# Kernel optimization log

Measured on AMD Instinct MI355X. Metric: run time of the kernel, lower is better.

Reference implementation:

```python
import jax, jax.numpy as jnp
import numpy as np

IN_DIM = 1024
HID = 256
OUT_DIM = 1000
NUM_BINS = 51
BATCH = 2048
N_LEGAL = 200


def setup_inputs() -> dict:
    key = jax.random.key(0)
    ks = jax.random.split(key, 12)
    s = lambda fan_in: 1.0 / np.sqrt(fan_in)
    u = lambda k, shp, b: jax.random.uniform(k, shp, jnp.float32, -b, b)
    return {
        "x": jax.random.normal(ks[0], (BATCH, IN_DIM), jnp.float32),
        # weights stored as [in, out] (math-equivalent to torch Linear)
        "w_in": u(ks[1], (IN_DIM, HID), s(IN_DIM)),
        "b_in": u(ks[2], (HID,), s(IN_DIM)),
        "w_ah": u(ks[3], (HID, HID), s(HID)),
        "b_ah": u(ks[4], (HID,), s(HID)),
        "w_ao": u(ks[5], (HID, OUT_DIM * NUM_BINS), s(HID)),
        "b_ao": u(ks[6], (OUT_DIM * NUM_BINS,), s(HID)),
        "w_vh": u(ks[7], (HID, HID), s(HID)),
        "b_vh": u(ks[8], (HID,), s(HID)),
        "w_vo": u(ks[9], (HID, NUM_BINS), s(HID)),
        "b_vo": u(ks[10], (NUM_BINS,), s(HID)),
        "v_range": jnp.linspace(-10.0, 10.0, NUM_BINS, dtype=jnp.float32),
        "possible_moves": jax.random.randint(ks[11], (BATCH, N_LEGAL), 0, OUT_DIM),
    }


def reference(x, w_in, b_in, w_ah, b_ah, w_ao, b_ao, w_vh, b_vh, w_vo, b_vo,
              v_range, possible_moves):
    B = x.shape[0]
    h = jax.nn.relu(x @ w_in + b_in)                       # [B, 256]
    adv_h = jax.nn.relu(h @ w_ah + b_ah)                   # [B, 256]
    val_h = jax.nn.relu(h @ w_vh + b_vh)                   # [B, 256]
    adv = (adv_h @ w_ao + b_ao).reshape(B, OUT_DIM, NUM_BINS)
    val = (val_h @ w_vo + b_vo).reshape(B, 1, NUM_BINS)
    q = val + adv - adv.mean(axis=1, keepdims=True)        # [B, A, bins]
    p = jnp.maximum(jax.nn.softmax(q, axis=2), 1e-5)       # softmax + clamp(min=1e-5)
    q_vals = jnp.sum(p * v_range, axis=2)                  # [B, A]
    # LegalSoftmax: per-row scatter of 1.0 at legal indices, vectorized
    mask = jnp.zeros((B, OUT_DIM), x.dtype).at[
        jnp.arange(B)[:, None], possible_moves].set(1.0)
    filtered = q_vals * mask
    # faithful to torch: any exact-zero entry (masked OR coincidental) -> -inf
    return jnp.where(filtered == 0, -jnp.inf, filtered)
```

## Files before the change

### kernel.cpp

```cpp
#include <hip/hip_runtime.h>
#include <cstdint>
#include <cstddef>

#define NB      2048
#define INDIM   1024
#define HID     256
#define NA      1000
#define BINS    51
#define NLEG    200
#define NPAIR   (NB*NLEG)
#define PPB     (NPAIR/256)
#define RSTRIDE 768

#define NEG_SENTINEL (-1.0e30f)

typedef float    f32x4  __attribute__((ext_vector_type(4)));
typedef __bf16   bf16x8 __attribute__((ext_vector_type(8)));
typedef unsigned short us8 __attribute__((ext_vector_type(8)));
typedef unsigned short us4 __attribute__((ext_vector_type(4)));
typedef unsigned long long u64x2 __attribute__((ext_vector_type(2)));

__device__ __forceinline__ unsigned short f2bf(float f) {
  union { float f; unsigned u; } v; v.f = f;
  return (unsigned short)((v.u + 0x7FFFu + ((v.u >> 16) & 1u)) >> 16);
}
__device__ __forceinline__ bf16x8 as_bf(us8 v) { return __builtin_bit_cast(bf16x8, v); }
__device__ __forceinline__ int imin(int a, int b) { return a < b ? a : b; }

__device__ __forceinline__ unsigned f2fp8x4(float a, float b, float c, float d) {
  int v = 0;
  v = __builtin_amdgcn_cvt_pk_fp8_f32(a, b, v, false);
  v = __builtin_amdgcn_cvt_pk_fp8_f32(c, d, v, true);
  return (unsigned)v;
}
__device__ __forceinline__ unsigned char f2fp8(float f) {
  int v = __builtin_amdgcn_cvt_pk_fp8_f32(f, 0.f, 0, false);
  return (unsigned char)(v & 0xff);
}
__device__ __forceinline__ float fp82f(unsigned char u) {
  return __builtin_amdgcn_cvt_f32_fp8((int)u, 0);
}

__global__ __launch_bounds__(256) void k_pre(
    const float* __restrict__ w_ao, unsigned char* __restrict__ wp8,
    float* __restrict__ wmean_acc,
    const float* __restrict__ w_in, const float* __restrict__ w_ah,
    const float* __restrict__ w_vh,
    unsigned short* __restrict__ w_inT, unsigned short* __restrict__ w_ahT,
    unsigned short* __restrict__ w_vhT,
    float* __restrict__ out,
    const float* __restrict__ x, unsigned short* __restrict__ x_bf) {
  __shared__ __align__(16) unsigned char smem[16320];
  int b = blockIdx.x, tid = threadIdx.x;
  if (b < 1000) {
    unsigned char* st = smem;
    int s = b & 7, a0 = (b >> 3) * 8;
    const float* wbase = w_ao + (size_t)(s * 32) * (NA * BINS) + a0 * BINS;
    for (int i = tid; i < 816; i += 256) {
      int kq = i / 102, c4 = i - kq * 102;
      const float* rp = wbase + (size_t)(kq * 4) * (NA * BINS) + c4 * 4;
      float4 f0 = *(const float4*)(rp);
      float4 f1 = *(const float4*)(rp + NA * BINS);
      float4 f2 = *(const float4*)(rp + 2 * NA * BINS);
      float4 f3 = *(const float4*)(rp + 3 * NA * BINS);
      unsigned pk0 = f2fp8x4(f0.x * 16.f, f0.y * 16.f, f0.z * 16.f, f0.w * 16.f);
      unsigned pk1 = f2fp8x4(f1.x * 16.f, f1.y * 16.f, f1.z * 16.f, f1.w * 16.f);
      unsigned pk2 = f2fp8x4(f2.x * 16.f, f2.y * 16.f, f2.z * 16.f, f2.w * 16.f);
      unsigned pk3 = f2fp8x4(f3.x * 16.f, f3.y * 16.f, f3.z * 16.f, f3.w * 16.f);
      unsigned s01lo = __builtin_amdgcn_perm(pk1, pk0, 0x05010400u);
      unsigned s01hi = __builtin_amdgcn_perm(pk1, pk0, 0x07030602u);
      unsigned s23lo = __builtin_amdgcn_perm(pk3, pk2, 0x05010400u);
      unsigned s23hi = __builtin_amdgcn_perm(pk3, pk2, 0x07030602u);
      unsigned o0 = __builtin_amdgcn_perm(s23lo, s01lo, 0x05040100u);
      unsigned o1 = __builtin_amdgcn_perm(s23lo, s01lo, 0x07060302u);
      unsigned o2 = __builtin_amdgcn_perm(s23hi, s01hi, 0x05040100u);
      unsigned o3 = __builtin_amdgcn_perm(s23hi, s01hi, 0x07060302u);
      int k4 = kq * 4;
      int swz = ((c4 >> 2) & 3) << 3;
      int kb = ((k4 & 24) ^ swz) + (k4 & 7);
      int cbase = c4 * 160;
      *(unsigned*)(st + cbase + kb)       = o0;
      *(unsigned*)(st + cbase + 40 + kb)  = o1;
      *(unsigned*)(st + cbase + 80 + kb)  = o2;
      *(unsigned*)(st + cbase + 120 + kb) = o3;
    }
    __syncthreads();
    for (int i = tid; i < 32 * 51; i += 256) {
      int r = i / 51, j = i - r * 51;
      float s8 = 0.f;
#pragma unroll
      for (int aL = 0; aL < 8; aL++) {
        int c = aL * 51 + j;
        s8 += fp82f(st[c * 40 + ((r & 24) ^ (((c >> 4) & 3) << 3)) + (r & 7)]);
      }
      atomicAdd(&wmean_acc[(size_t)(s * 32 + r) * BINS + j], s8);
    }
    int t4 = (tid >> 6) & 3, l = tid & 63;
    int col = t4 * 16 + (l & 15), kg = l >> 4;
    for (int aL = 0; aL < 8; aL++) {
      unsigned lo = 0, hi = 0;
      if (col < BINS) {
        int ci = aL * 51 + col;
        unsigned long long v8 = *(const unsigned long long*)(
            st + ci * 40 + ((kg * 8) ^ (((ci >> 4) & 3) << 3)));
        lo = (unsigned)v8; hi = (unsigned)(v8 >> 32);
      }
      uint2 v; v.x = lo; v.y = hi;
      *(uint2*)(wp8 + (size_t)(a0 + aL) * 16384 +
                (size_t)((s * 2 + (t4 >> 1)) * 64 + l) * 16 + (t4 & 1) * 8) = v;
    }
  } else if (b < 1384) {
    int bb = b - 1000;
    float (*tile)[33] = (float(*)[33])smem;
    const float* w; unsigned short* wT; int K, N, kt, nt;
    if (bb < 256)      { w = w_in; wT = w_inT; K = INDIM; N = HID; kt = bb & 31;        nt = bb >> 5; }
    else if (bb < 320) { w = w_ah; wT = w_ahT; K = HID;   N = HID; kt = (bb - 256) & 7; nt = (bb - 256) >> 3; }
    else               { w = w_vh; wT = w_vhT; K = HID;   N = HID; kt = (bb - 320) & 7; nt = (bb - 320) >> 3; }
    int k0 = kt * 32, n0 = nt * 32;
    int cr = tid >> 5, cc = tid & 31;
#pragma unroll
    for (int it = 0; it < 4; it++)
      tile[cr + it * 8][cc] = w[(size_t)(k0 + cr + it * 8) * N + n0 + cc];
    __syncthreads();
#pragma unroll
    for (int it = 0; it < 4; it++)
      wT[(size_t)(n0 + cr + it * 8) * K + k0 + cc] = f2bf(tile[cc][cr + it * 8]);
  } else if (b < 1884) {
    int base = (b - 1384) * 1024 + tid;
    float4 v = {NEG_SENTINEL, NEG_SENTINEL, NEG_SENTINEL, NEG_SENTINEL};
#pragma unroll
    for (int it = 0; it < 4; it++) ((float4*)out)[base + it * 256] = v;
  } else {
    int base4 = (b - 1884) * 1024 + tid;
#pragma unroll
    for (int it = 0; it < 4; it++) {
      float4 v = ((const float4*)x)[base4 + it * 256];
      us4 o;
      o[0] = f2bf(v.x); o[1] = f2bf(v.y); o[2] = f2bf(v.z); o[3] = f2bf(v.w);
      ((us4*)x_bf)[base4 + it * 256] = o;
    }
  }
}

__global__ __launch_bounds__(256) void k_mid(
    const unsigned short* __restrict__ x_bf, const unsigned short* __restrict__ w_inT,
    const float* __restrict__ b_in, unsigned short* __restrict__ h_bf,
    const float* __restrict__ w_vo, const float* __restrict__ wmean_acc,
    const float* __restrict__ b_vo, const float* __restrict__ b_ao,
    unsigned short* __restrict__ Wc, float* __restrict__ bias_c) {
  __shared__ __align__(16) char smem[1024];
  int b = blockIdx.x, tid = threadIdx.x;
  if (b < 512) {
    int w = tid >> 6, l = tid & 63, la = l & 15, g = l >> 4;
    int idx = b * 4 + w;
    int m0 = (idx & 127) * 16, n0 = (idx >> 7) * 16;
    f32x4 acc = {0.f, 0.f, 0.f, 0.f};
    const us8* Bp = (const us8*)(w_inT + (size_t)(n0 + la) * INDIM) + g;
    const us8* Ap = (const us8*)(x_bf + (size_t)(m0 + la) * INDIM) + g;
#pragma unroll 8
    for (int s = 0; s < 32; s++)
      acc = __builtin_amdgcn_mfma_f32_16x16x32_bf16(as_bf(Ap[s * 4]), as_bf(Bp[s * 4]),
                                                    acc, 0, 0, 0);
    float bb = b_in[n0 + la];
#pragma unroll
    for (int r = 0; r < 4; r++) {
      float v = fmaxf(acc[r] + bb, 0.f);
      h_bf[(size_t)(m0 + g * 4 + r) * HID + n0 + la] = f2bf(v);
    }
  } else {
    float* sred = (float*)smem;
    int n = b - 512, t = tid;
    for (int k = t; k < 512; k += 256) {
      float v = 0.f;
      if (n < BINS)
        v = (k < 256) ? w_vo[(size_t)k * BINS + n]
                      : (-(0.001f / 16.f) * wmean_acc[(size_t)(k - 256) * BINS + n]);
      Wc[(size_t)n * 512 + k] = f2bf(v);
    }
    float acc = 0.f;
    if (n < BINS)
      for (int a = t; a < NA; a += 256) acc += b_ao[(size_t)a * BINS + n];
    sred[t] = acc;
    __syncthreads();
    for (int d = 128; d > 0; d >>= 1) { if (t < d) sred[t] += sred[t + d]; __syncthreads(); }
    if (t == 0) bias_c[n] = (n < BINS) ? (b_vo[n] - 0.001f * sred[0]) : 0.f;
  }
}

__global__ __launch_bounds__(256) void k_heads(
    const unsigned short* __restrict__ h,
    const unsigned short* __restrict__ wA, const float* __restrict__ bA,
    const unsigned short* __restrict__ wV, const float* __restrict__ bV,
    const unsigned short* __restrict__ Wc, const float* __restrict__ bias_c,
    unsigned char* __restrict__ Aext8, float* __restrict__ cbuf_f,
    const int* __restrict__ pm, int* __restrict__ cursor, int* __restrict__ rows) {
  __shared__ __align__(16) char smem[16896];
  int b = blockIdx.x, tid = threadIdx.x;
  if (b < 128) {
    unsigned short* aL = (unsigned short*)smem;
    unsigned short* vL = (unsigned short*)smem + 16 * 264;
    int w = tid >> 6, l = tid & 63, la = l & 15, g = l >> 4;
    int m0 = b * 16;
    const us8* Ap = (const us8*)(h + (size_t)(m0 + la) * HID) + g;
    us8 aF[8];
#pragma unroll
    for (int s = 0; s < 8; s++) aF[s] = Ap[s * 4];
#pragma unroll
    for (int part = 0; part < 2; part++) {
      const unsigned short* BT = part ? wV : wA;
      const float* bias = part ? bV : bA;
      unsigned short* oL = part ? vL : aL;
#pragma unroll
      for (int nt = 0; nt < 4; nt++) {
        int n0 = w * 64 + nt * 16;
        f32x4 acc = {0.f, 0.f, 0.f, 0.f};
        const us8* Bp = (const us8*)(BT + (size_t)(n0 + la) * HID) + g;
#pragma unroll
        for (int s = 0; s < 8; s++)
          acc = __builtin_amdgcn_mfma_f32_16x16x32_bf16(as_bf(aF[s]), as_bf(Bp[s * 4]),
                                                        acc, 0, 0, 0);
        float bb = bias[n0 + la];
#pragma unroll
        for (int r = 0; r < 4; r++) {
          float v = fmaxf(acc[r] + bb, 0.f);
          oL[(g * 4 + r) * 264 + n0 + la] = f2bf(v);
          if (part == 0)
            Aext8[(size_t)(m0 + g * 4 + r) * HID + n0 + la] = f2fp8(v);
        }
      }
    }
    __syncthreads();
    int n0c = w * 16;
    f32x4 acc = {0.f, 0.f, 0.f, 0.f};
    const us8* Vp  = (const us8*)(vL + la * 264) + g;
    const us8* Ap2 = (const us8*)(aL + la * 264) + g;
    const us8* BpV = (const us8*)(Wc + (size_t)(n0c + la) * 512) + g;
    const us8* BpA = (const us8*)(Wc + (size_t)(n0c + la) * 512 + 256) + g;
#pragma unroll
    for (int s = 0; s < 8; s++)
      acc = __builtin_amdgcn_mfma_f32_16x16x32_bf16(as_bf(Vp[s * 4]), as_bf(BpV[s * 4]),
                                                    acc, 0, 0, 0);
#pragma unroll
    for (int s = 0; s < 8; s++)
      acc = __builtin_amdgcn_mfma_f32_16x16x32_bf16(as_bf(Ap2[s * 4]), as_bf(BpA[s * 4]),
                                                    acc, 0, 0, 0);
    float bb = bias_c[n0c + la];
#pragma unroll
    for (int r = 0; r < 4; r++)
      cbuf_f[(size_t)(m0 + g * 4 + r) * 64 + n0c + la] = acc[r] + bb;
  } else {
    int* lc = (int*)smem;
    int* lbase = (int*)(smem + 4096);
    int blk = b - 128, t = tid;
    for (int i = t; i < NA; i += 256) lc[i] = 0;
    __syncthreads();
    int pbase = blk * PPB;
    for (int i = t; i < PPB; i += 256) atomicAdd(&lc[pm[pbase + i]], 1);
    __syncthreads();
    for (int i = t; i < NA; i += 256) {
      int v = lc[i];
      lbase[i] = v ? atomicAdd(&cursor[i], v) : 0;
      lc[i] = 0;
    }
    __syncthreads();
    for (int i = t; i < PPB; i += 256) {
      int a = pm[pbase + i];
      int r = atomicAdd(&lc[a], 1);
      rows[(size_t)a * RSTRIDE + lbase[a] + r] = (pbase + i) / NLEG;
    }
  }
}

#define TILE_BODY(TILE, RA_) do {                                              \
  int rA = (RA_);                                                              \
  const long long* Ap = (const long long*)(Aext8 + (size_t)rA * HID) + g;      \
  const float4* cf = (const float4*)(cbuf_f + (size_t)rA * 64);                \
  long long a8[8];                                                             \
  _Pragma("unroll") for (int s = 0; s < 8; s++) a8[s] = Ap[s * 4];             \
  float4 cq0 = cf[g], cq1 = cf[4 + g], cq2 = cf[8 + g], cq3 = cf[12 + g];      \
  f32x4 acc0 = {0.f,0.f,0.f,0.f}, acc1 = {0.f,0.f,0.f,0.f};                    \
  f32x4 acc2 = {0.f,0.f,0.f,0.f}, acc3 = {0.f,0.f,0.f,0.f};                    \
  __builtin_amdgcn_s_setprio(1);                                               \
  _Pragma("unroll") for (int s = 0; s < 8; s++) {                              \
    u64x2 b01 = sBv[(s * 2) * 64 + l];                                         \
    u64x2 b23 = sBv[(s * 2 + 1) * 64 + l];                                     \
    acc0 = __builtin_amdgcn_mfma_f32_16x16x32_fp8_fp8(                         \
        (long long)b01[0], a8[s], acc0, 0, 0, 0);                              \
    acc1 = __builtin_amdgcn_mfma_f32_16x16x32_fp8_fp8(                         \
        (long long)b01[1], a8[s], acc1, 0, 0, 0);                              \
    acc2 = __builtin_amdgcn_mfma_f32_16x16x32_fp8_fp8(                         \
        (long long)b23[0], a8[s], acc2, 0, 0, 0);                              \
    acc3 = __builtin_amdgcn_mfma_f32_16x16x32_fp8_fp8(                         \
        (long long)b23[1], a8[s], acc3, 0, 0, 0);                              \
  }                                                                            \
  __builtin_amdgcn_s_setprio(0);                                               \
  float S = 0.f;                                                               \
  f32x4 e0, e1, e2, e3;                                                        \
  _Pragma("unroll") for (int r = 0; r < 4; r++) {                              \
    e0[r] = __expf(fmaf(acc0[r], 0.0625f, cq0[r] + bao0[r])); S += e0[r];      \
    e1[r] = __expf(fmaf(acc1[r], 0.0625f, cq1[r] + bao1[r])); S += e1[r];      \
    e2[r] = __expf(fmaf(acc2[r], 0.0625f, cq2[r] + bao2[r])); S += e2[r];      \
    e3[r] = __expf(fmaf(acc3[r], 0.0625f, cq3[r] + bao3[r])); S += e3[r];      \
  }                                                                            \
  S += __shfl_xor(S, 16); S += __shfl_xor(S, 32);                              \
  float inv = 1.f / S, qv = 0.f;                                               \
  _Pragma("unroll") for (int r = 0; r < 4; r++) {                              \
    int bin = g * 4 + r;                                                       \
    qv = fmaf(fmaxf(e0[r] * inv, 1e-5f), (float)bin * 0.4f - 10.f, qv);        \
    qv = fmaf(fmaxf(e1[r] * inv, 1e-5f), (float)(bin + 16) * 0.4f - 10.f, qv); \
    qv = fmaf(fmaxf(e2[r] * inv, 1e-5f), (float)(bin + 32) * 0.4f - 10.f, qv); \
    if (bin + 48 < BINS)                                                       \
      qv = fmaf(fmaxf(e3[r] * inv, 1e-5f), (float)(bin + 48) * 0.4f - 10.f, qv); \
  }                                                                            \
  qv += __shfl_xor(qv, 16); qv += __shfl_xor(qv, 32);                          \
  int gi = (TILE) * 16 + la;                                                   \
  if (g == 0 && gi < count)                                                    \
    out[(size_t)rA * NA + a] = (qv == 0.f) ? NEG_SENTINEL : qv;                \
} while (0)

__global__ __launch_bounds__(256) void k_main_mfma(
    const unsigned char* __restrict__ Aext8,
    const float* __restrict__ cbuf_f,
    const unsigned char* __restrict__ wp8,
    const float* __restrict__ b_ao,
    const int* __restrict__ cnt,
    const int* __restrict__ rows,
    float* __restrict__ out) {
  __shared__ __align__(16) long long sB8[2048];
  const u64x2* sBv = (const u64x2*)sB8;
  int bx = blockIdx.x;
  int a = (bx & 7) * 125 + (bx >> 3);
  int count = cnt[a];
  int ntiles = (count + 15) >> 4;
  if (count == 0 || (int)(blockIdx.y * 4) >= ntiles) return;
  int tid = threadIdx.x;
  int w = tid >> 6, l = tid & 63, la = l & 15, g = l >> 4;
  int base = a * RSTRIDE;
  int t0 = blockIdx.y * 4 + w;

  int rQ0 = rows[base + imin( t0       * 16 + la, count - 1)];
  int rQ1 = rows[base + imin((t0 +  8) * 16 + la, count - 1)];
  int rQ2 = rows[base + imin((t0 + 16) * 16 + la, count - 1)];
  int rQ3 = rows[base + imin((t0 + 24) * 16 + la, count - 1)];

  const float* baop = b_ao + (size_t)a * BINS;
  f32x4 bao0, bao1, bao2, bao3;
#pragma unroll
  for (int r = 0; r < 4; r++) {
    int bin = g * 4 + r;
    bao0[r] = baop[bin];
    bao1[r] = baop[bin + 16];
    bao2[r] = baop[bin + 32];
    bao3[r] = (bin + 48 < BINS) ? baop[bin + 48] : NEG_SENTINEL;
  }

  const u64x2* wpa = (const u64x2*)(wp8 + (size_t)a * 16384);
#pragma unroll
  for (int i = 0; i < 4; i++) ((u64x2*)sB8)[tid + i * 256] = wpa[tid + i * 256];
  __syncthreads();

  if (t0      < ntiles) TILE_BODY(t0,      rQ0);
  if (t0 +  8 < ntiles) TILE_BODY(t0 +  8, rQ1);
  if (t0 + 16 < ntiles) TILE_BODY(t0 + 16, rQ2);
  if (t0 + 24 < ntiles) TILE_BODY(t0 + 24, rQ3);
  for (int tile = t0 + 32; tile < ntiles; tile += 8) {
    int rAt = rows[base + imin(tile * 16 + la, count - 1)];
    TILE_BODY(tile, rAt);
  }
}

extern "C" void kernel_launch(void* const* d_in, const int* in_sizes, int n_in,
                              void* d_out, int out_size, void* d_ws, size_t ws_size,
                              hipStream_t stream) {
  (void)in_sizes; (void)n_in; (void)out_size; (void)ws_size;
  const float* x     = (const float*)d_in[0];
  const float* w_in  = (const float*)d_in[1];
  const float* b_in  = (const float*)d_in[2];
  const float* w_ah  = (const float*)d_in[3];
  const float* b_ah  = (const float*)d_in[4];
  const float* w_ao  = (const float*)d_in[5];
  const float* b_ao  = (const float*)d_in[6];
  const float* w_vh  = (const float*)d_in[7];
  const float* b_vh  = (const float*)d_in[8];
  const float* w_vo  = (const float*)d_in[9];
  const float* b_vo  = (const float*)d_in[10];
  const int*   pm    = (const int*)d_in[12];
  float* out = (float*)d_out;

  char* p = (char*)d_ws;
  unsigned char*  wp8    = (unsigned char*)p;  p += (size_t)NA * 32 * 512;
  unsigned char*  Aext8  = (unsigned char*)p;  p += (size_t)NB * HID;
  unsigned short* h_bf   = (unsigned short*)p; p += (size_t)NB * HID * 2;
  unsigned short* w_inT  = (unsigned short*)p; p += (size_t)HID * INDIM * 2;
  unsigned short* w_ahT  = (unsigned short*)p; p += (size_t)HID * HID * 2;
  unsigned short* w_vhT  = (unsigned short*)p; p += (size_t)HID * HID * 2;
  unsigned short* Wc     = (unsigned short*)p; p += (size_t)64 * 512 * 2;
  unsigned short* x_bf   = (unsigned short*)p; p += (size_t)NB * INDIM * 2;
  float* bias_c = (float*)p; p += 64 * 4;
  float* cbuf_f = (float*)p; p += (size_t)NB * 64 * 4;
  float* wmean  = (float*)p; p += 13056 * 4;
  int* cursor = (int*)p; p += (size_t)NA * 4 + 240;
  int* rows   = (int*)p; p += (size_t)NA * RSTRIDE * 4 + 256;

  hipMemsetAsync(wmean, 0, (13056 + NA) * sizeof(float), stream);

  k_pre<<<2396, 256, 0, stream>>>(w_ao, wp8, wmean, w_in, w_ah, w_vh,
                                  w_inT, w_ahT, w_vhT, out, x, x_bf);
  k_mid<<<576, 256, 0, stream>>>(x_bf, w_inT, b_in, h_bf,
                                 w_vo, wmean, b_vo, b_ao, Wc, bias_c);
  k_heads<<<384, 256, 0, stream>>>(h_bf, w_ahT, b_ah, w_vhT, b_vh,
                                   Wc, bias_c, Aext8, cbuf_f,
                                   pm, cursor, rows);
  k_main_mfma<<<dim3(1000, 2), 256, 0, stream>>>(Aext8, cbuf_f, wp8, b_ao,
                                                 cursor, rows, out);
}
```

Before: 201.1 us.

## Spread column-mean atomics over slices and double-buffer row prefetch in main kernel

The weight-column-mean accumulation in k_pre now spreads its atomics across 25 partial buffers by slice, so fewer blocks contend on the same addresses. k_mid then sums the 25 slices when it builds Wc. In k_main_mfma the per-tile body is split into a prefetch macro and a compute macro, with two register sets (A/B), so the next tile's gathered A rows and cbuf loads are issued before the current tile's MFMA and softmax. This costs a larger memset and workspace, more reads in k_mid, and higher register pressure in the main kernel.

```diff
diff --git a/kernel.cpp b/kernel.cpp
--- a/kernel.cpp
+++ b/kernel.cpp
@@ -11,6 +11,7 @@
 #define NPAIR   (NB*NLEG)
 #define PPB     (NPAIR/256)
 #define RSTRIDE 768
+#define NSLICE  25
 
 #define NEG_SENTINEL (-1.0e30f)
 
@@ -43,7 +44,7 @@
 
 __global__ __launch_bounds__(256) void k_pre(
     const float* __restrict__ w_ao, unsigned char* __restrict__ wp8,
-    float* __restrict__ wmean_acc,
+    float* __restrict__ wpart,
     const float* __restrict__ w_in, const float* __restrict__ w_ah,
     const float* __restrict__ w_vh,
     unsigned short* __restrict__ w_inT, unsigned short* __restrict__ w_ahT,
@@ -85,6 +86,7 @@
       *(unsigned*)(st + cbase + 120 + kb) = o3;
     }
     __syncthreads();
+    int slice = (b >> 3) % NSLICE;
     for (int i = tid; i < 32 * 51; i += 256) {
       int r = i / 51, j = i - r * 51;
       float s8 = 0.f;
@@ -93,7 +95,7 @@
         int c = aL * 51 + j;
         s8 += fp82f(st[c * 40 + ((r & 24) ^ (((c >> 4) & 3) << 3)) + (r & 7)]);
       }
-      atomicAdd(&wmean_acc[(size_t)(s * 32 + r) * BINS + j], s8);
+      atomicAdd(&wpart[(size_t)slice * 13056 + (s * 32 + r) * 51 + j], s8);
     }
     int t4 = (tid >> 6) & 3, l = tid & 63;
     int col = t4 * 16 + (l & 15), kg = l >> 4;
@@ -145,7 +147,7 @@
 __global__ __launch_bounds__(256) void k_mid(
     const unsigned short* __restrict__ x_bf, const unsigned short* __restrict__ w_inT,
     const float* __restrict__ b_in, unsigned short* __restrict__ h_bf,
-    const float* __restrict__ w_vo, const float* __restrict__ wmean_acc,
+    const float* __restrict__ w_vo, const float* __restrict__ wpart,
     const float* __restrict__ b_vo, const float* __restrict__ b_ao,
     unsigned short* __restrict__ Wc, float* __restrict__ bias_c) {
   __shared__ __align__(16) char smem[1024];
@@ -172,9 +174,17 @@
     int n = b - 512, t = tid;
     for (int k = t; k < 512; k += 256) {
       float v = 0.f;
-      if (n < BINS)
-        v = (k < 256) ? w_vo[(size_t)k * BINS + n]
-                      : (-(0.001f / 16.f) * wmean_acc[(size_t)(k - 256) * BINS + n]);
+      if (n < BINS) {
+        if (k < 256) {
+          v = w_vo[(size_t)k * BINS + n];
+        } else {
+          float ssum = 0.f;
+#pragma unroll
+          for (int sl = 0; sl < NSLICE; sl++)
+            ssum += wpart[(size_t)sl * 13056 + (k - 256) * 51 + n];
+          v = -(0.001f / 16.f) * ssum;
+        }
+      }
       Wc[(size_t)n * 512 + k] = f2bf(v);
     }
     float acc = 0.f;
@@ -271,51 +281,58 @@
   }
 }
 
-#define TILE_BODY(TILE, RA_) do {                                              \
-  int rA = (RA_);                                                              \
-  const long long* Ap = (const long long*)(Aext8 + (size_t)rA * HID) + g;      \
-  const float4* cf = (const float4*)(cbuf_f + (size_t)rA * 64);                \
-  long long a8[8];                                                             \
-  _Pragma("unroll") for (int s = 0; s < 8; s++) a8[s] = Ap[s * 4];             \
-  float4 cq0 = cf[g], cq1 = cf[4 + g], cq2 = cf[8 + g], cq3 = cf[12 + g];      \
-  f32x4 acc0 = {0.f,0.f,0.f,0.f}, acc1 = {0.f,0.f,0.f,0.f};                    \
-  f32x4 acc2 = {0.f,0.f,0.f,0.f}, acc3 = {0.f,0.f,0.f,0.f};                    \
+#define PREF(P, RA_) do {                                                      \
+  rA##P = (RA_);                                                               \
+  const long long* Ap_ = (const long long*)(Aext8 + (size_t)rA##P * HID) + g;  \
+  a##P##0 = Ap_[0];  a##P##1 = Ap_[4];  a##P##2 = Ap_[8];  a##P##3 = Ap_[12];  \
+  a##P##4 = Ap_[16]; a##P##5 = Ap_[20]; a##P##6 = Ap_[24]; a##P##7 = Ap_[28];  \
+  const float4* cf_ = (const float4*)(cbuf_f + (size_t)rA##P * 64);            \
+  cq##P##0 = cf_[g];     cq##P##1 = cf_[4 + g];                                \
+  cq##P##2 = cf_[8 + g]; cq##P##3 = cf_[12 + g];                               \
+} while (0)
+
+#define MSTEP(P, S) do {                                                       \
+  u64x2 b01_ = sBv[(S * 2) * 64 + l];                                          \
+  u64x2 b23_ = sBv[(S * 2 + 1) * 64 + l];                                      \
+  acc0_ = __builtin_amdgcn_mfma_f32_16x16x32_fp8_fp8(                          \
+      (long long)b01_[0], a##P##S, acc0_, 0, 0, 0);                            \
+  acc1_ = __builtin_amdgcn_mfma_f32_16x16x32_fp8_fp8(                          \
+      (long long)b01_[1], a##P##S, acc1_, 0, 0, 0);                            \
+  acc2_ = __builtin_amdgcn_mfma_f32_16x16x32_fp8_fp8(                          \
+      (long long)b23_[0], a##P##S, acc2_, 0, 0, 0);                            \
+  acc3_ = __builtin_amdgcn_mfma_f32_16x16x32_fp8_fp8(                          \
+      (long long)b23_[1], a##P##S, acc3_, 0, 0, 0);                            \
+} while (0)
+
+#define COMP(P, TILE) do {                                                     \
+  f32x4 acc0_ = {0.f,0.f,0.f,0.f}, acc1_ = {0.f,0.f,0.f,0.f};                  \
+  f32x4 acc2_ = {0.f,0.f,0.f,0.f}, acc3_ = {0.f,0.f,0.f,0.f};                  \
   __builtin_amdgcn_s_setprio(1);                                               \
-  _Pragma("unroll") for (int s = 0; s < 8; s++) {                              \
-    u64x2 b01 = sBv[(s * 2) * 64 + l];                                         \
-    u64x2 b23 = sBv[(s * 2 + 1) * 64 + l];                                     \
-    acc0 = __builtin_amdgcn_mfma_f32_16x16x32_fp8_fp8(                         \
-        (long long)b01[0], a8[s], acc0, 0, 0, 0);                              \
-    acc1 = __builtin_amdgcn_mfma_f32_16x16x32_fp8_fp8(                         \
-        (long long)b01[1], a8[s], acc1, 0, 0, 0);                              \
-    acc2 = __builtin_amdgcn_mfma_f32_16x16x32_fp8_fp8(                         \
-        (long long)b23[0], a8[s], acc2, 0, 0, 0);                              \
-    acc3 = __builtin_amdgcn_mfma_f32_16x16x32_fp8_fp8(                         \
-        (long long)b23[1], a8[s], acc3, 0, 0, 0);                              \
+  MSTEP(P, 0); MSTEP(P, 1); MSTEP(P, 2); MSTEP(P, 3);                          \
+  MSTEP(P, 4); MSTEP(P, 5); MSTEP(P, 6); MSTEP(P, 7);                          \
+  __builtin_amdgcn_s_setprio(0);                                               \
+  float S_ = 0.f;                                                              \
+  f32x4 e0_, e1_, e2_, e3_;                                                    \
+  _Pragma("unroll") for (int r_ = 0; r_ < 4; r_++) {                           \
+    e0_[r_] = __expf(fmaf(acc0_[r_], 0.0625f, cq##P##0[r_] + bao0[r_])); S_ += e0_[r_]; \
+    e1_[r_] = __expf(fmaf(acc1_[r_], 0.0625f, cq##P##1[r_] + bao1[r_])); S_ += e1_[r_]; \
+    e2_[r_] = __expf(fmaf(acc2_[r_], 0.0625f, cq##P##2[r_] + bao2[r_])); S_ += e2_[r_]; \
+    e3_[r_] = __expf(fmaf(acc3_[r_], 0.0625f, cq##P##3[r_] + bao3[r_])); S_ += e3_[r_]; \
   }                                                                            \
-  __builtin_amdgcn_s_setprio(0);                                               \
-  float S = 0.f;                                                               \
-  f32x4 e0, e1, e2, e3;                                                        \
-  _Pragma("unroll") for (int r = 0; r < 4; r++) {                              \
-    e0[r] = __expf(fmaf(acc0[r], 0.0625f, cq0[r] + bao0[r])); S += e0[r];      \
-    e1[r] = __expf(fmaf(acc1[r], 0.0625f, cq1[r] + bao1[r])); S += e1[r];      \
-    e2[r] = __expf(fmaf(acc2[r], 0.0625f, cq2[r] + bao2[r])); S += e2[r];      \
-    e3[r] = __expf(fmaf(acc3[r], 0.0625f, cq3[r] + bao3[r])); S += e3[r];      \
+  S_ += __shfl_xor(S_, 16); S_ += __shfl_xor(S_, 32);                          \
+  float inv_ = 1.f / S_, qv_ = 0.f;                                            \
+  _Pragma("unroll") for (int r_ = 0; r_ < 4; r_++) {                           \
+    int bin_ = g * 4 + r_;                                                     \
+    qv_ = fmaf(fmaxf(e0_[r_] * inv_, 1e-5f), (float)bin_ * 0.4f - 10.f, qv_);  \
+    qv_ = fmaf(fmaxf(e1_[r_] * inv_, 1e-5f), (float)(bin_ + 16) * 0.4f - 10.f, qv_); \
+    qv_ = fmaf(fmaxf(e2_[r_] * inv_, 1e-5f), (float)(bin_ + 32) * 0.4f - 10.f, qv_); \
+    if (bin_ + 48 < BINS)                                                      \
+      qv_ = fmaf(fmaxf(e3_[r_] * inv_, 1e-5f), (float)(bin_ + 48) * 0.4f - 10.f, qv_); \
   }                                                                            \
-  S += __shfl_xor(S, 16); S += __shfl_xor(S, 32);                              \
-  float inv = 1.f / S, qv = 0.f;                                               \
-  _Pragma("unroll") for (int r = 0; r < 4; r++) {                              \
-    int bin = g * 4 + r;                                                       \
-    qv = fmaf(fmaxf(e0[r] * inv, 1e-5f), (float)bin * 0.4f - 10.f, qv);        \
-    qv = fmaf(fmaxf(e1[r] * inv, 1e-5f), (float)(bin + 16) * 0.4f - 10.f, qv); \
-    qv = fmaf(fmaxf(e2[r] * inv, 1e-5f), (float)(bin + 32) * 0.4f - 10.f, qv); \
-    if (bin + 48 < BINS)                                                       \
-      qv = fmaf(fmaxf(e3[r] * inv, 1e-5f), (float)(bin + 48) * 0.4f - 10.f, qv); \
-  }                                                                            \
-  qv += __shfl_xor(qv, 16); qv += __shfl_xor(qv, 32);                          \
-  int gi = (TILE) * 16 + la;                                                   \
-  if (g == 0 && gi < count)                                                    \
-    out[(size_t)rA * NA + a] = (qv == 0.f) ? NEG_SENTINEL : qv;                \
+  qv_ += __shfl_xor(qv_, 16); qv_ += __shfl_xor(qv_, 32);                      \
+  int gi_ = (TILE) * 16 + la;                                                  \
+  if (g == 0 && gi_ < count)                                                   \
+    out[(size_t)rA##P * NA + a] = (qv_ == 0.f) ? NEG_SENTINEL : qv_;           \
 } while (0)
 
 __global__ __launch_bounds__(256) void k_main_mfma(
@@ -359,13 +376,26 @@
   for (int i = 0; i < 4; i++) ((u64x2*)sB8)[tid + i * 256] = wpa[tid + i * 256];
   __syncthreads();
 
-  if (t0      < ntiles) TILE_BODY(t0,      rQ0);
-  if (t0 +  8 < ntiles) TILE_BODY(t0 +  8, rQ1);
-  if (t0 + 16 < ntiles) TILE_BODY(t0 + 16, rQ2);
-  if (t0 + 24 < ntiles) TILE_BODY(t0 + 24, rQ3);
+  int rAA, rAB;
+  long long aA0, aA1, aA2, aA3, aA4, aA5, aA6, aA7;
+  long long aB0, aB1, aB2, aB3, aB4, aB5, aB6, aB7;
+  float4 cqA0, cqA1, cqA2, cqA3;
+  float4 cqB0, cqB1, cqB2, cqB3;
+  bool e0 = t0 < ntiles, e1 = t0 + 8 < ntiles,
+       e2 = t0 + 16 < ntiles, e3 = t0 + 24 < ntiles;
+
+  if (e0) PREF(A, rQ0);
+  if (e1) PREF(B, rQ1);
+  if (e0) COMP(A, t0);
+  if (e2) PREF(A, rQ2);
+  if (e1) COMP(B, t0 + 8);
+  if (e3) PREF(B, rQ3);
+  if (e2) COMP(A, t0 + 16);
+  if (e3) COMP(B, t0 + 24);
   for (int tile = t0 + 32; tile < ntiles; tile += 8) {
     int rAt = rows[base + imin(tile * 16 + la, count - 1)];
-    TILE_BODY(tile, rAt);
+    PREF(A, rAt);
+    COMP(A, tile);
   }
 }
 
@@ -398,16 +428,16 @@
   unsigned short* x_bf   = (unsigned short*)p; p += (size_t)NB * INDIM * 2;
   float* bias_c = (float*)p; p += 64 * 4;
   float* cbuf_f = (float*)p; p += (size_t)NB * 64 * 4;
-  float* wmean  = (float*)p; p += 13056 * 4;
+  float* wpart  = (float*)p; p += (size_t)NSLICE * 13056 * 4;
   int* cursor = (int*)p; p += (size_t)NA * 4 + 240;
   int* rows   = (int*)p; p += (size_t)NA * RSTRIDE * 4 + 256;
 
-  hipMemsetAsync(wmean, 0, (13056 + NA) * sizeof(float), stream);
-
-  k_pre<<<2396, 256, 0, stream>>>(w_ao, wp8, wmean, w_in, w_ah, w_vh,
+  hipMemsetAsync(wpart, 0, ((size_t)NSLICE * 13056 + NA) * sizeof(float), stream);
+
+  k_pre<<<2396, 256, 0, stream>>>(w_ao, wp8, wpart, w_in, w_ah, w_vh,
                                   w_inT, w_ahT, w_vhT, out, x, x_bf);
   k_mid<<<576, 256, 0, stream>>>(x_bf, w_inT, b_in, h_bf,
-                                 w_vo, wmean, b_vo, b_ao, Wc, bias_c);
+                                 w_vo, wpart, b_vo, b_ao, Wc, bias_c);
   k_heads<<<384, 256, 0, stream>>>(h_bf, w_ahT, b_ah, w_vhT, b_vh,
                                    Wc, bias_c, Aext8, cbuf_f,
                                    pm, cursor, rows);
```

After: 206.5 us. 2.7% more time.

## Replace wmean atomics with bf16 partials, move row bucketing into k_pre

Applied to the files above, without the earlier changes.

The column-mean accumulation of w_ao no longer uses global float atomics. Each block group writes bf16 partial sums to a buffer, and k_mid reduces the 125 partials. The legal-move bucketing (cursor/rows) moves from k_heads into k_pre so it overlaps with weight conversion. The output sentinel fill becomes a byte memset of 0xFE, which gives a large negative float instead of a kernel fill. This trades atomic contention for extra partial traffic, and the bf16 partials add rounding error to the mean correction.

```diff
diff --git a/kernel.cpp b/kernel.cpp
--- a/kernel.cpp
+++ b/kernel.cpp
@@ -24,6 +24,10 @@
   union { float f; unsigned u; } v; v.f = f;
   return (unsigned short)((v.u + 0x7FFFu + ((v.u >> 16) & 1u)) >> 16);
 }
+__device__ __forceinline__ float bf2f(unsigned short h) {
+  union { unsigned u; float f; } v; v.u = ((unsigned)h) << 16;
+  return v.f;
+}
 __device__ __forceinline__ bf16x8 as_bf(us8 v) { return __builtin_bit_cast(bf16x8, v); }
 __device__ __forceinline__ int imin(int a, int b) { return a < b ? a : b; }
 
@@ -43,13 +47,14 @@
 
 __global__ __launch_bounds__(256) void k_pre(
     const float* __restrict__ w_ao, unsigned char* __restrict__ wp8,
-    float* __restrict__ wmean_acc,
+    unsigned short* __restrict__ wpart,
     const float* __restrict__ w_in, const float* __restrict__ w_ah,
     const float* __restrict__ w_vh,
     unsigned short* __restrict__ w_inT, unsigned short* __restrict__ w_ahT,
     unsigned short* __restrict__ w_vhT,
-    float* __restrict__ out,
-    const float* __restrict__ x, unsigned short* __restrict__ x_bf) {
+    const float* __restrict__ x, unsigned short* __restrict__ x_bf,
+    const int* __restrict__ pm, int* __restrict__ cursor,
+    int* __restrict__ rows) {
   __shared__ __align__(16) unsigned char smem[16320];
   int b = blockIdx.x, tid = threadIdx.x;
   if (b < 1000) {
@@ -85,6 +90,7 @@
       *(unsigned*)(st + cbase + 120 + kb) = o3;
     }
     __syncthreads();
+    unsigned short* wp = wpart + (size_t)(b >> 3) * 13056;
     for (int i = tid; i < 32 * 51; i += 256) {
       int r = i / 51, j = i - r * 51;
       float s8 = 0.f;
@@ -93,7 +99,7 @@
         int c = aL * 51 + j;
         s8 += fp82f(st[c * 40 + ((r & 24) ^ (((c >> 4) & 3) << 3)) + (r & 7)]);
       }
-      atomicAdd(&wmean_acc[(size_t)(s * 32 + r) * BINS + j], s8);
+      wp[(s * 32 + r) * 51 + j] = f2bf(s8);
     }
     int t4 = (tid >> 6) & 3, l = tid & 63;
     int col = t4 * 16 + (l & 15), kg = l >> 4;
@@ -125,13 +131,8 @@
 #pragma unroll
     for (int it = 0; it < 4; it++)
       wT[(size_t)(n0 + cr + it * 8) * K + k0 + cc] = f2bf(tile[cc][cr + it * 8]);
-  } else if (b < 1884) {
-    int base = (b - 1384) * 1024 + tid;
-    float4 v = {NEG_SENTINEL, NEG_SENTINEL, NEG_SENTINEL, NEG_SENTINEL};
-#pragma unroll
-    for (int it = 0; it < 4; it++) ((float4*)out)[base + it * 256] = v;
-  } else {
-    int base4 = (b - 1884) * 1024 + tid;
+  } else if (b < 1896) {
+    int base4 = (b - 1384) * 1024 + tid;
 #pragma unroll
     for (int it = 0; it < 4; it++) {
       float4 v = ((const float4*)x)[base4 + it * 256];
@@ -139,13 +140,33 @@
       o[0] = f2bf(v.x); o[1] = f2bf(v.y); o[2] = f2bf(v.z); o[3] = f2bf(v.w);
       ((us4*)x_bf)[base4 + it * 256] = o;
     }
+  } else {
+    int* lc = (int*)smem;
+    int* lbase = (int*)(smem + 4096);
+    int blk = b - 1896, t = tid;
+    for (int i = t; i < NA; i += 256) lc[i] = 0;
+    __syncthreads();
+    int pbase = blk * PPB;
+    for (int i = t; i < PPB; i += 256) atomicAdd(&lc[pm[pbase + i]], 1);
+    __syncthreads();
+    for (int i = t; i < NA; i += 256) {
+      int v = lc[i];
+      lbase[i] = v ? atomicAdd(&cursor[i], v) : 0;
+      lc[i] = 0;
+    }
+    __syncthreads();
+    for (int i = t; i < PPB; i += 256) {
+      int a = pm[pbase + i];
+      int r = atomicAdd(&lc[a], 1);
+      rows[(size_t)a * RSTRIDE + lbase[a] + r] = (pbase + i) / NLEG;
+    }
   }
 }
 
 __global__ __launch_bounds__(256) void k_mid(
     const unsigned short* __restrict__ x_bf, const unsigned short* __restrict__ w_inT,
     const float* __restrict__ b_in, unsigned short* __restrict__ h_bf,
-    const float* __restrict__ w_vo, const float* __restrict__ wmean_acc,
+    const float* __restrict__ w_vo, const unsigned short* __restrict__ wpart,
     const float* __restrict__ b_vo, const float* __restrict__ b_ao,
     unsigned short* __restrict__ Wc, float* __restrict__ bias_c) {
   __shared__ __align__(16) char smem[1024];
@@ -172,9 +193,18 @@
     int n = b - 512, t = tid;
     for (int k = t; k < 512; k += 256) {
       float v = 0.f;
-      if (n < BINS)
-        v = (k < 256) ? w_vo[(size_t)k * BINS + n]
-                      : (-(0.001f / 16.f) * wmean_acc[(size_t)(k - 256) * BINS + n]);
+      if (n < BINS) {
+        if (k < 256) {
+          v = w_vo[(size_t)k * BINS + n];
+        } else {
+          float ssum = 0.f;
+          const unsigned short* wp = wpart + (size_t)(k - 256) * 51 + n;
+#pragma unroll 8
+          for (int sl = 0; sl < 125; sl++)
+            ssum += bf2f(wp[(size_t)sl * 13056]);
+          v = -(0.001f / 16.f) * ssum;
+        }
+      }
       Wc[(size_t)n * 512 + k] = f2bf(v);
     }
     float acc = 0.f;
@@ -192,83 +222,59 @@
     const unsigned short* __restrict__ wA, const float* __restrict__ bA,
     const unsigned short* __restrict__ wV, const float* __restrict__ bV,
     const unsigned short* __restrict__ Wc, const float* __restrict__ bias_c,
-    unsigned char* __restrict__ Aext8, float* __restrict__ cbuf_f,
-    const int* __restrict__ pm, int* __restrict__ cursor, int* __restrict__ rows) {
-  __shared__ __align__(16) char smem[16896];
+    unsigned char* __restrict__ Aext8, float* __restrict__ cbuf_f) {
+  __shared__ __align__(16) unsigned short aL[16 * 264];
+  __shared__ __align__(16) unsigned short vL[16 * 264];
   int b = blockIdx.x, tid = threadIdx.x;
-  if (b < 128) {
-    unsigned short* aL = (unsigned short*)smem;
-    unsigned short* vL = (unsigned short*)smem + 16 * 264;
-    int w = tid >> 6, l = tid & 63, la = l & 15, g = l >> 4;
-    int m0 = b * 16;
-    const us8* Ap = (const us8*)(h + (size_t)(m0 + la) * HID) + g;
-    us8 aF[8];
-#pragma unroll
-    for (int s = 0; s < 8; s++) aF[s] = Ap[s * 4];
-#pragma unroll
-    for (int part = 0; part < 2; part++) {
-      const unsigned short* BT = part ? wV : wA;
-      const float* bias = part ? bV : bA;
-      unsigned short* oL = part ? vL : aL;
-#pragma unroll
-      for (int nt = 0; nt < 4; nt++) {
-        int n0 = w * 64 + nt * 16;
-        f32x4 acc = {0.f, 0.f, 0.f, 0.f};
-        const us8* Bp = (const us8*)(BT + (size_t)(n0 + la) * HID) + g;
-#pragma unroll
-        for (int s = 0; s < 8; s++)
-          acc = __builtin_amdgcn_mfma_f32_16x16x32_bf16(as_bf(aF[s]), as_bf(Bp[s * 4]),
-                                                        acc, 0, 0, 0);
-        float bb = bias[n0 + la];
-#pragma unroll
-        for (int r = 0; r < 4; r++) {
-          float v = fmaxf(acc[r] + bb, 0.f);
-          oL[(g * 4 + r) * 264 + n0 + la] = f2bf(v);
-          if (part == 0)
-            Aext8[(size_t)(m0 + g * 4 + r) * HID + n0 + la] = f2fp8(v);
-        }
+  int w = tid >> 6, l = tid & 63, la = l & 15, g = l >> 4;
+  int m0 = b * 16;
+  const us8* Ap = (const us8*)(h + (size_t)(m0 + la) * HID) + g;
+  us8 aF[8];
+#pragma unroll
+  for (int s = 0; s < 8; s++) aF[s] = Ap[s * 4];
+#pragma unroll
+  for (int part = 0; part < 2; part++) {
+    const unsigned short* BT = part ? wV : wA;
+    const float* bias = part ? bV : bA;
+    unsigned short* oL = part ? vL : aL;
+#pragma unroll
+    for (int nt = 0; nt < 4; nt++) {
+      int n0 = w * 64 + nt * 16;
+      f32x4 acc = {0.f, 0.f, 0.f, 0.f};
+      const us8* Bp = (const us8*)(BT + (size_t)(n0 + la) * HID) + g;
+#pragma unroll
+      for (int s = 0; s < 8; s++)
+        acc = __builtin_amdgcn_mfma_f32_16x16x32_bf16(as_bf(aF[s]), as_bf(Bp[s * 4]),
+                                                      acc, 0, 0, 0);
+      float bb = bias[n0 + la];
+#pragma unroll
+      for (int r = 0; r < 4; r++) {
+        float v = fmaxf(acc[r] + bb, 0.f);
+        oL[(g * 4 + r) * 264 + n0 + la] = f2bf(v);
+        if (part == 0)
+          Aext8[(size_t)(m0 + g * 4 + r) * HID + n0 + la] = f2fp8(v);
       }
     }
-    __syncthreads();
-    int n0c = w * 16;
-    f32x4 acc = {0.f, 0.f, 0.f, 0.f};
-    const us8* Vp  = (const us8*)(vL + la * 264) + g;
-    const us8* Ap2 = (const us8*)(aL + la * 264) + g;
-    const us8* BpV = (const us8*)(Wc + (size_t)(n0c + la) * 512) + g;
-    const us8* BpA = (const us8*)(Wc + (size_t)(n0c + la) * 512 + 256) + g;
-#pragma unroll
-    for (int s = 0; s < 8; s++)
-      acc = __builtin_amdgcn_mfma_f32_16x16x32_bf16(as_bf(Vp[s * 4]), as_bf(BpV[s * 4]),
-                                                    acc, 0, 0, 0);
-#pragma unroll
-    for (int s = 0; s < 8; s++)
-      acc = __builtin_amdgcn_mfma_f32_16x16x32_bf16(as_bf(Ap2[s * 4]), as_bf(BpA[s * 4]),
-                                                    acc, 0, 0, 0);
-    float bb = bias_c[n0c + la];
-#pragma unroll
-    for (int r = 0; r < 4; r++)
-      cbuf_f[(size_t)(m0 + g * 4 + r) * 64 + n0c + la] = acc[r] + bb;
-  } else {
-    int* lc = (int*)smem;
-    int* lbase = (int*)(smem + 4096);
-    int blk = b - 128, t = tid;
-    for (int i = t; i < NA; i += 256) lc[i] = 0;
-    __syncthreads();
-    int pbase = blk * PPB;
-    for (int i = t; i < PPB; i += 256) atomicAdd(&lc[pm[pbase + i]], 1);
-    __syncthreads();
-    for (int i = t; i < NA; i += 256) {
-      int v = lc[i];
-      lbase[i] = v ? atomicAdd(&cursor[i], v) : 0;
-      lc[i] = 0;
-    }
-    __syncthreads();
-    for (int i = t; i < PPB; i += 256) {
-      int a = pm[pbase + i];
-      int r = atomicAdd(&lc[a], 1);
-      rows[(size_t)a * RSTRIDE + lbase[a] + r] = (pbase + i) / NLEG;
-    }
   }
+  __syncthreads();
+  int n0c = w * 16;
+  f32x4 acc = {0.f, 0.f, 0.f, 0.f};
+  const us8* Vp  = (const us8*)(vL + la * 264) + g;
+  const us8* Ap2 = (const us8*)(aL + la * 264) + g;
+  const us8* BpV = (const us8*)(Wc + (size_t)(n0c + la) * 512) + g;
+  const us8* BpA = (const us8*)(Wc + (size_t)(n0c + la) * 512 + 256) + g;
+#pragma unroll
+  for (int s = 0; s < 8; s++)
+    acc = __builtin_amdgcn_mfma_f32_16x16x32_bf16(as_bf(Vp[s * 4]), as_bf(BpV[s * 4]),
+                                                  acc, 0, 0, 0);
+#pragma unroll
+  for (int s = 0; s < 8; s++)
+    acc = __builtin_amdgcn_mfma_f32_16x16x32_bf16(as_bf(Ap2[s * 4]), as_bf(BpA[s * 4]),
+                                                  acc, 0, 0, 0);
+  float bb = bias_c[n0c + la];
+#pragma unroll
+  for (int r = 0; r < 4; r++)
+    cbuf_f[(size_t)(m0 + g * 4 + r) * 64 + n0c + la] = acc[r] + bb;
 }
 
 #define TILE_BODY(TILE, RA_) do {                                              \
@@ -398,19 +404,20 @@
   unsigned short* x_bf   = (unsigned short*)p; p += (size_t)NB * INDIM * 2;
   float* bias_c = (float*)p; p += 64 * 4;
   float* cbuf_f = (float*)p; p += (size_t)NB * 64 * 4;
-  float* wmean  = (float*)p; p += 13056 * 4;
+  unsigned short* wpart = (unsigned short*)p; p += (size_t)125 * 13056 * 2;
   int* cursor = (int*)p; p += (size_t)NA * 4 + 240;
   int* rows   = (int*)p; p += (size_t)NA * RSTRIDE * 4 + 256;
 
-  hipMemsetAsync(wmean, 0, (13056 + NA) * sizeof(float), stream);
-
-  k_pre<<<2396, 256, 0, stream>>>(w_ao, wp8, wmean, w_in, w_ah, w_vh,
-                                  w_inT, w_ahT, w_vhT, out, x, x_bf);
+  hipMemsetAsync(cursor, 0, NA * sizeof(int), stream);
+  hipMemsetAsync(out, 0xFE, (size_t)NB * NA * sizeof(float), stream);
+
+  k_pre<<<2152, 256, 0, stream>>>(w_ao, wp8, wpart, w_in, w_ah, w_vh,
+                                  w_inT, w_ahT, w_vhT, x, x_bf,
+                                  pm, cursor, rows);
   k_mid<<<576, 256, 0, stream>>>(x_bf, w_inT, b_in, h_bf,
-                                 w_vo, wmean, b_vo, b_ao, Wc, bias_c);
-  k_heads<<<384, 256, 0, stream>>>(h_bf, w_ahT, b_ah, w_vhT, b_vh,
-                                   Wc, bias_c, Aext8, cbuf_f,
-                                   pm, cursor, rows);
+                                 w_vo, wpart, b_vo, b_ao, Wc, bias_c);
+  k_heads<<<128, 256, 0, stream>>>(h_bf, w_ahT, b_ah, w_vhT, b_vh,
+                                   Wc, bias_c, Aext8, cbuf_f);
   k_main_mfma<<<dim3(1000, 2), 256, 0, stream>>>(Aext8, cbuf_f, wp8, b_ao,
                                                  cursor, rows, out);
 }
```

New measurement: 225.7 us. 1.12x slower.
